# Performance work log

Measured on AMD Instinct MI355X. Metric: run time of the kernel, lower is better.

The kernel has to match this reference:

```python
import jax, jax.numpy as jnp
import numpy as np

KS = 5          # kernel_size
D = 2           # spatial dim
DX = 0.01       # region kernel spacing
SCALE = 1.0
NX, NY = 32, 32
N = NX * NY


def _region_kernel():
    # gaussians.region_kernel: KS x KS grid of offsets spaced DX, centered at 0
    off = (jnp.arange(KS, dtype=jnp.float32) - (KS - 1) / 2.0) * DX
    gx, gy = jnp.meshgrid(off, off, indexing='ij')
    return jnp.stack([gx, gy], -1).reshape(-1, D)  # (KS*KS, 2)


def _build_cov(scaling, transform):
    # Cholesky-style parameterization: L lower-triangular with diag=scaling,
    # off-diag=transform; cov = L @ L^T (d=2 closed form)
    s0, s1 = scaling[:, 0], scaling[:, 1]
    t = transform[:, 0]
    c00 = s0 * s0
    c01 = s0 * t
    c11 = t * t + s1 * s1
    return jnp.stack([jnp.stack([c00, c01], -1), jnp.stack([c01, c11], -1)], -2)


def _inv2x2(c):
    det = c[:, 0, 0] * c[:, 1, 1] - c[:, 0, 1] * c[:, 1, 0]
    inv = jnp.stack([jnp.stack([c[:, 1, 1], -c[:, 0, 1]], -1),
                     jnp.stack([-c[:, 1, 0], c[:, 0, 0]], -1)], -2)
    return inv / det[:, None, None]


def setup_inputs() -> dict:
    key = jax.random.key(0)
    ks = jax.random.split(key, 20)
    # Gaussian state: grid means as in __init__
    tx = jnp.linspace(-1.0, 1.0, NX) * SCALE
    ty = jnp.linspace(-1.0, 1.0, NY) * SCALE
    gx, gy = jnp.meshgrid(tx, ty, indexing='ij')
    means = jnp.stack([gx, gy], -1).reshape(-1, D).astype(jnp.float32)
    u = 0.1 * jax.random.normal(ks[0], (N, 1), jnp.float32)
    scaling = jnp.exp(-4.5 + 0.2 * jax.random.normal(ks[1], (N, D), jnp.float32)) * SCALE
    transform = 0.002 * jax.random.normal(ks[2], (N, 1), jnp.float32)
    opacities = 2.0 + 0.1 * jax.random.normal(ks[3], (N,), jnp.float32)
    # network weights (4 heads share the first 3 layer shapes)
    convW = 0.05 * jax.random.normal(ks[4], (4, 50, 3, KS, KS), jnp.float32)
    convb = 0.01 * jax.random.normal(ks[5], (4, 50), jnp.float32)
    embW = 0.3 * jax.random.normal(ks[6], (4, 7, 30), jnp.float32)
    embb = 0.01 * jax.random.normal(ks[7], (4, 30), jnp.float32)
    l1W = 0.1 * jax.random.normal(ks[8], (4, 80, 80), jnp.float32)
    l1b = 0.01 * jax.random.normal(ks[9], (4, 80), jnp.float32)
    outW_sol = 0.1 * jax.random.normal(ks[10], (80, 1), jnp.float32)
    outb_sol = 0.01 * jax.random.normal(ks[11], (1,), jnp.float32)
    outW_trans = 0.1 * jax.random.normal(ks[12], (80, 2), jnp.float32)
    outb_trans = 0.01 * jax.random.normal(ks[13], (2,), jnp.float32)
    outW_scale = 0.1 * jax.random.normal(ks[14], (80, 2), jnp.float32)
    outb_scale = 0.01 * jax.random.normal(ks[15], (2,), jnp.float32)
    outW_tform = 0.1 * jax.random.normal(ks[16], (80, 1), jnp.float32)
    outb_tform = 0.01 * jax.random.normal(ks[17], (1,), jnp.float32)
    return {"means": means, "u": u, "scaling": scaling, "transform": transform,
            "opacities": opacities, "convW": convW, "convb": convb,
            "embW": embW, "embb": embb, "l1W": l1W, "l1b": l1b,
            "outW_sol": outW_sol, "outb_sol": outb_sol,
            "outW_trans": outW_trans, "outb_trans": outb_trans,
            "outW_scale": outW_scale, "outb_scale": outb_scale,
            "outW_tform": outW_tform, "outb_tform": outb_tform}


def reference(means, u, scaling, transform, opacities, convW, convb, embW, embb,
              l1W, l1b, outW_sol, outb_sol, outW_trans, outb_trans,
              outW_scale, outb_scale, outW_tform, outb_tform):
    n = means.shape[0]
    cov = _build_cov(scaling, transform)          # (N,2,2)
    conics = _inv2x2(cov)                         # (N,2,2)

    # --- sampling (torch.no_grad block in original) ---
    kern = _region_kernel()                                        # (25,2)
    samples = (means[:, None, :] + kern[None]).reshape(-1, D)      # (M,2), M=N*25
    bc = jnp.all(jnp.abs(samples) < SCALE, -1).astype(means.dtype)[:, None]
    alpha = jax.nn.sigmoid(opacities)                              # (N,)
    diff = samples[:, None, :] - means[None, :, :]                 # (M,N,2)
    Cq = jnp.einsum('nij,mnj->mni', conics, diff)                  # (M,N,2)
    G = jnp.exp(-0.5 * jnp.einsum('mni,mni->mn', diff, Cq)) * alpha[None, :]  # (M,N)
    u_s = G @ u                                                    # (M,1)
    # DIFFUSION pde_rhs = trace of laplacian: sum_n G * (|C q|^2 - tr(C)) * u_n
    trC = conics[:, 0, 0] + conics[:, 1, 1]
    lap = jnp.einsum('mn,mn,nc->mc', G, (Cq ** 2).sum(-1) - trC[None, :], u)  # (M,1)
    in_samples = jax.lax.stop_gradient(jnp.concatenate([u_s, lap, bc], -1))   # (M,3)

    # (N, 25, 3) -> (N, 3, 5, 5)
    img = in_samples.reshape(n, KS * KS, -1).transpose(0, 2, 1).reshape(n, -1, KS, KS)
    in_params = jnp.concatenate([means, u, scaling, transform, opacities[:, None]], -1)  # (N,7)

    # 4 Networks: conv(5x5 -> 1x1, 50ch) + param embed(7->30) + MLP(80->80->out)
    y = jnp.tanh(jnp.einsum('ncij,kocij->kno', img, convW) + convb[:, None, :])   # (4,N,50)
    e = jnp.tanh(jnp.einsum('nf,kfg->kng', in_params, embW) + embb[:, None, :])   # (4,N,30)
    h = jnp.tanh(jnp.einsum('knf,kfg->kng', jnp.concatenate([y, e], -1), l1W)
                 + l1b[:, None, :])                                               # (4,N,80)

    deltas = h[0] @ outW_sol + outb_sol          # (N,1)
    translation = h[1] @ outW_trans + outb_trans # (N,2)
    dscale = h[2] @ outW_scale + outb_scale      # (N,2)
    dtransform = h[3] @ outW_tform + outb_tform  # (N,1)

    u_new = u + deltas
    means_new = means + translation
    scaling_new = scaling * jnp.exp(dscale)
    transform_new = transform + dtransform
    cov_new = _build_cov(scaling_new, transform_new)
    return (u_new, means_new, scaling_new, transform_new, cov_new)
```

## Files before the change

### kernel.cpp

```cpp
#include <hip/hip_runtime.h>
#include <hip/hip_bf16.h>


#define NG 1024

__global__ __launch_bounds__(256) void k_fused(
    const float* __restrict__ means, const float* __restrict__ u,
    const float* __restrict__ scal, const float* __restrict__ trans,
    const float* __restrict__ opac,
    const float* __restrict__ convW, const float* __restrict__ convb,
    const float* __restrict__ embW,  const float* __restrict__ embb,
    const float* __restrict__ l1W,   const float* __restrict__ l1b,
    const float* __restrict__ oWs,  const float* __restrict__ obs,
    const float* __restrict__ oWt,  const float* __restrict__ obt,
    const float* __restrict__ oWsc, const float* __restrict__ obsc,
    const float* __restrict__ oWtf, const float* __restrict__ obtf,
    float* __restrict__ out)
{
    __shared__ float gd[NG * 8];
    __shared__ float pus[8][32];
    __shared__ float plap[8][32];
    __shared__ float simg[80];
    __shared__ float hin[4][80];
    __shared__ float hv[4][80];
    __shared__ float outs[8];

    const int t = threadIdx.x;
    const int n = blockIdx.x;

    for (int g = t; g < NG; g += 256) {
        float gmx = means[2*g], gmy = means[2*g+1];
        float s0  = scal[2*g],  s1  = scal[2*g+1];
        float tt  = trans[g];
        float c00 = s0*s0, c01 = s0*tt, c11 = tt*tt + s1*s1;
        float idet = 1.0f / (c00*c11 - c01*c01);
        float A = c11*idet, B = -c01*idet, C = c00*idet;
        float alpha = 1.0f / (1.0f + __expf(-opac[g]));
        float4* dst = (float4*)(gd + g*8);
        dst[0] = make_float4(gmx, gmy, A, B);
        dst[1] = make_float4(C, A + C, alpha * u[g], 0.0f);
    }
    __syncthreads();

    const float mx = means[2*n], my = means[2*n+1];

    {
        int s = t & 31, c = t >> 5;
        if (s < 25) {
            int si = s / 5, sj = s - si * 5;
            float sx = mx + (float)(si - 2) * 0.01f;
            float sy = my + (float)(sj - 2) * 0.01f;
            float us = 0.0f, lp = 0.0f;
            const float* gp = gd + c * 128 * 8;
            #pragma unroll 4
            for (int i = 0; i < 128; ++i) {
                float4 a = *(const float4*)(gp + i*8);
                float4 b = *(const float4*)(gp + i*8 + 4);
                float dx = sx - a.x, dy = sy - a.y;
                float Cq0 = a.z*dx + a.w*dy;
                float Cq1 = a.w*dx + b.x*dy;
                float q   = dx*Cq0 + dy*Cq1;
                float e   = __expf(-0.5f*q) * b.z;
                us += e;
                lp += e * (Cq0*Cq0 + Cq1*Cq1 - b.y);
            }
            pus[c][s] = us; plap[c][s] = lp;
        }
    }
    __syncthreads();

    if (t < 25) {
        float us = 0.0f, lp = 0.0f;
        #pragma unroll
        for (int c = 0; c < 8; ++c) { us += pus[c][t]; lp += plap[c][t]; }
        int si = t / 5, sj = t - si * 5;
        float sx = mx + (float)(si - 2) * 0.01f;
        float sy = my + (float)(sj - 2) * 0.01f;
        simg[t]      = us;
        simg[25 + t] = lp;
        simg[50 + t] = (fabsf(sx) < 1.0f && fabsf(sy) < 1.0f) ? 1.0f : 0.0f;
    }
    __syncthreads();

    if (t < 200) {
        int k = t / 50, o = t - k * 50;
        const float* w = convW + (size_t)(k * 50 + o) * 75;
        float acc = convb[k * 50 + o];
        #pragma unroll 5
        for (int j = 0; j < 75; ++j) acc += simg[j] * w[j];
        hin[k][o] = tanhf(acc);
    } else {
        float inp[7] = { mx, my, u[n], scal[2*n], scal[2*n+1], trans[n], opac[n] };
        for (int idx = t - 200; idx < 120; idx += 56) {
            int k = idx / 30, g = idx - k * 30;
            float acc = embb[k * 30 + g];
            #pragma unroll
            for (int f = 0; f < 7; ++f) acc += inp[f] * embW[(k*7 + f)*30 + g];
            hin[k][50 + g] = tanhf(acc);
        }
    }
    __syncthreads();

    for (int idx = t; idx < 320; idx += 256) {
        int k = idx / 80, g = idx - k * 80;
        float acc = l1b[k * 80 + g];
        #pragma unroll 8
        for (int f = 0; f < 80; ++f)
            acc += hin[k][f] * l1W[(k*80 + f)*80 + g];
        hv[k][g] = tanhf(acc);
    }
    __syncthreads();

    if (t < 6) {
        const float* W; const float* bb; int k, j, stride;
        if (t == 0)      { W = oWs;  bb = obs;  k = 0; j = 0;     stride = 1; }
        else if (t < 3)  { W = oWt;  bb = obt;  k = 1; j = t - 1; stride = 2; }
        else if (t < 5)  { W = oWsc; bb = obsc; k = 2; j = t - 3; stride = 2; }
        else             { W = oWtf; bb = obtf; k = 3; j = 0;     stride = 1; }
        float acc = bb[j];
        #pragma unroll 8
        for (int f = 0; f < 80; ++f) acc += hv[k][f] * W[f * stride + j];
        outs[t] = acc;
    }
    __syncthreads();

    if (t == 0) {
        float uu = u[n];
        float s0 = scal[2*n], s1 = scal[2*n+1];
        float tr = trans[n];
        float u_new = uu + outs[0];
        float mxn = mx + outs[1], myn = my + outs[2];
        float s0n = s0 * expf(outs[3]);
        float s1n = s1 * expf(outs[4]);
        float tn  = tr + outs[5];
        float c00 = s0n*s0n, c01 = s0n*tn, c11 = tn*tn + s1n*s1n;
        out[n]              = u_new;
        out[1024 + 2*n]     = mxn;
        out[1024 + 2*n + 1] = myn;
        out[3072 + 2*n]     = s0n;
        out[3072 + 2*n + 1] = s1n;
        out[5120 + n]       = tn;
        out[6144 + 4*n]     = c00;
        out[6144 + 4*n + 1] = c01;
        out[6144 + 4*n + 2] = c01;
        out[6144 + 4*n + 3] = c11;
    }
}

extern "C" void kernel_launch(void* const* d_in, const int* in_sizes, int n_in,
                              void* d_out, int out_size, void* d_ws, size_t ws_size,
                              hipStream_t stream)
{
    k_fused<<<dim3(NG), dim3(256), 0, stream>>>(
        (const float*)d_in[0],  (const float*)d_in[1],  (const float*)d_in[2],
        (const float*)d_in[3],  (const float*)d_in[4],  (const float*)d_in[5],
        (const float*)d_in[6],  (const float*)d_in[7],  (const float*)d_in[8],
        (const float*)d_in[9],  (const float*)d_in[10], (const float*)d_in[11],
        (const float*)d_in[12], (const float*)d_in[13], (const float*)d_in[14],
        (const float*)d_in[15], (const float*)d_in[16], (const float*)d_in[17],
        (const float*)d_in[18], (float*)d_out);
}
```

Baseline: 120.5 us.

## Cull distant gaussians per block and precompute gaussian params in prep kernel

```diff
diff --git a/kernel.cpp b/kernel.cpp
--- a/kernel.cpp
+++ b/kernel.cpp
@@ -3,46 +3,78 @@
 
 
 #define NG 1024
+#define WS_GD   0
+#define WS_CWT  (NG * 8)
+
+__global__ __launch_bounds__(256) void k_prep(
+    const float* __restrict__ means, const float* __restrict__ u,
+    const float* __restrict__ scal,  const float* __restrict__ trans,
+    const float* __restrict__ opac,  const float* __restrict__ convW,
+    float* __restrict__ ws)
+{
+    int gid = blockIdx.x * 256 + threadIdx.x;
+    if (gid < NG) {
+        float gmx = means[2*gid], gmy = means[2*gid+1];
+        float s0  = scal[2*gid],  s1  = scal[2*gid+1];
+        float tt  = trans[gid];
+        float c00 = s0*s0, c01 = s0*tt, c11 = tt*tt + s1*s1;
+        float idet = 1.0f / (c00*c11 - c01*c01);
+        float A = c11*idet, B = -c01*idet, C = c00*idet;
+        float alpha = 1.0f / (1.0f + __expf(-opac[gid]));
+        float r2 = 100.0f * (c00 + c11);
+        float4* dst = (float4*)(ws + WS_GD + gid*8);
+        dst[0] = make_float4(gmx, gmy, A, B);
+        dst[1] = make_float4(C, A + C, alpha * u[gid], r2);
+    }
+    float* wt = ws + WS_CWT;
+    for (int idx = gid; idx < 15000; idx += gridDim.x * 256) {
+        int ko = idx / 75, j = idx - ko * 75;
+        wt[j * 200 + ko] = convW[idx];
+    }
+}
 
 __global__ __launch_bounds__(256) void k_fused(
     const float* __restrict__ means, const float* __restrict__ u,
     const float* __restrict__ scal, const float* __restrict__ trans,
     const float* __restrict__ opac,
-    const float* __restrict__ convW, const float* __restrict__ convb,
+    const float* __restrict__ convb,
     const float* __restrict__ embW,  const float* __restrict__ embb,
     const float* __restrict__ l1W,   const float* __restrict__ l1b,
     const float* __restrict__ oWs,  const float* __restrict__ obs,
     const float* __restrict__ oWt,  const float* __restrict__ obt,
     const float* __restrict__ oWsc, const float* __restrict__ obsc,
     const float* __restrict__ oWtf, const float* __restrict__ obtf,
+    const float* __restrict__ ws,
     float* __restrict__ out)
 {
-    __shared__ float gd[NG * 8];
+    __shared__ float gcomp[NG * 8];
     __shared__ float pus[8][32];
     __shared__ float plap[8][32];
     __shared__ float simg[80];
     __shared__ float hin[4][80];
     __shared__ float hv[4][80];
     __shared__ float outs[8];
+    __shared__ int   cnt;
 
     const int t = threadIdx.x;
     const int n = blockIdx.x;
-
+    const float mx = means[2*n], my = means[2*n+1];
+
+    if (t == 0) cnt = 0;
+    __syncthreads();
     for (int g = t; g < NG; g += 256) {
-        float gmx = means[2*g], gmy = means[2*g+1];
-        float s0  = scal[2*g],  s1  = scal[2*g+1];
-        float tt  = trans[g];
-        float c00 = s0*s0, c01 = s0*tt, c11 = tt*tt + s1*s1;
-        float idet = 1.0f / (c00*c11 - c01*c01);
-        float A = c11*idet, B = -c01*idet, C = c00*idet;
-        float alpha = 1.0f / (1.0f + __expf(-opac[g]));
-        float4* dst = (float4*)(gd + g*8);
-        dst[0] = make_float4(gmx, gmy, A, B);
-        dst[1] = make_float4(C, A + C, alpha * u[g], 0.0f);
-    }
-    __syncthreads();
-
-    const float mx = means[2*n], my = means[2*n+1];
+        const float4* src = (const float4*)(ws + WS_GD + g*8);
+        float4 a = src[0], b = src[1];
+        float ddx = fmaxf(fabsf(a.x - mx) - 0.02f, 0.0f);
+        float ddy = fmaxf(fabsf(a.y - my) - 0.02f, 0.0f);
+        if (ddx*ddx + ddy*ddy <= b.w) {
+            int slot = atomicAdd(&cnt, 1);
+            float4* dst = (float4*)(gcomp + slot*8);
+            dst[0] = a; dst[1] = b;
+        }
+    }
+    __syncthreads();
+    const int nsurv = cnt;
 
     {
         int s = t & 31, c = t >> 5;
@@ -51,11 +83,10 @@
             float sx = mx + (float)(si - 2) * 0.01f;
             float sy = my + (float)(sj - 2) * 0.01f;
             float us = 0.0f, lp = 0.0f;
-            const float* gp = gd + c * 128 * 8;
-            #pragma unroll 4
-            for (int i = 0; i < 128; ++i) {
-                float4 a = *(const float4*)(gp + i*8);
-                float4 b = *(const float4*)(gp + i*8 + 4);
+            #pragma unroll 2
+            for (int i = c; i < nsurv; i += 8) {
+                float4 a = *(const float4*)(gcomp + i*8);
+                float4 b = *(const float4*)(gcomp + i*8 + 4);
                 float dx = sx - a.x, dy = sy - a.y;
                 float Cq0 = a.z*dx + a.w*dy;
                 float Cq1 = a.w*dx + b.x*dy;
@@ -83,12 +114,11 @@
     __syncthreads();
 
     if (t < 200) {
-        int k = t / 50, o = t - k * 50;
-        const float* w = convW + (size_t)(k * 50 + o) * 75;
-        float acc = convb[k * 50 + o];
+        const float* wt = ws + WS_CWT;
+        float acc = convb[t];
         #pragma unroll 5
-        for (int j = 0; j < 75; ++j) acc += simg[j] * w[j];
-        hin[k][o] = tanhf(acc);
+        for (int j = 0; j < 75; ++j) acc += simg[j] * wt[j*200 + t];
+        hin[t / 50][t % 50] = tanhf(acc);
     } else {
         float inp[7] = { mx, my, u[n], scal[2*n], scal[2*n+1], trans[n], opac[n] };
         for (int idx = t - 200; idx < 120; idx += 56) {
@@ -151,12 +181,21 @@
                               void* d_out, int out_size, void* d_ws, size_t ws_size,
                               hipStream_t stream)
 {
+    const float* means = (const float*)d_in[0];
+    const float* u     = (const float*)d_in[1];
+    const float* scal  = (const float*)d_in[2];
+    const float* trans = (const float*)d_in[3];
+    const float* opac  = (const float*)d_in[4];
+    const float* convW = (const float*)d_in[5];
+    float* ws = (float*)d_ws;
+
+    k_prep<<<dim3(64), dim3(256), 0, stream>>>(means, u, scal, trans, opac,
+                                               convW, ws);
     k_fused<<<dim3(NG), dim3(256), 0, stream>>>(
-        (const float*)d_in[0],  (const float*)d_in[1],  (const float*)d_in[2],
-        (const float*)d_in[3],  (const float*)d_in[4],  (const float*)d_in[5],
+        means, u, scal, trans, opac,
         (const float*)d_in[6],  (const float*)d_in[7],  (const float*)d_in[8],
         (const float*)d_in[9],  (const float*)d_in[10], (const float*)d_in[11],
         (const float*)d_in[12], (const float*)d_in[13], (const float*)d_in[14],
         (const float*)d_in[15], (const float*)d_in[16], (const float*)d_in[17],
-        (const float*)d_in[18], (float*)d_out);
+        (const float*)d_in[18], ws, (float*)d_out);
 }
```

Measured after the change: 111.2 us. 7.7% less time.
